# Kernel optimization log

Hardware: AMD Instinct MI355X
Metric: run time of the kernel (lower is better)

Reference implementation:

```python
import jax, jax.numpy as jnp
import numpy as np

N_NODES = 100000
N_EDGES = 3200000
N_GRAPHS = 4096
N_REL = 5
N_BASES = 4
HID = 32


def setup_inputs() -> dict:
    key = jax.random.key(0)
    ks = jax.random.split(key, 32)
    inp = {}
    inp['x'] = jax.random.normal(ks[0], (N_NODES, 4), dtype=jnp.float32)
    inp['edge_index'] = jax.random.randint(ks[1], (2, N_EDGES), 0, N_NODES, dtype=jnp.int64)
    inp['edge_type'] = jax.random.randint(ks[2], (N_EDGES,), 0, N_REL, dtype=jnp.int64)
    inp['user_idx'] = jax.random.randint(ks[3], (N_GRAPHS,), 0, N_NODES, dtype=jnp.int64)
    inp['item_idx'] = jax.random.randint(ks[4], (N_GRAPHS,), 0, N_NODES, dtype=jnp.int64)
    k = 5
    for l in range(4):
        in_c = 4 if l == 0 else HID
        inp[f'basis{l}'] = jax.random.normal(ks[k], (N_BASES, in_c, HID), dtype=jnp.float32) * 0.1; k += 1
        inp[f'comp{l}'] = jax.random.normal(ks[k], (N_REL, N_BASES), dtype=jnp.float32) * 0.5; k += 1
        inp[f'root{l}'] = jax.random.normal(ks[k], (in_c, HID), dtype=jnp.float32) * 0.1; k += 1
        inp[f'bias{l}'] = jax.random.normal(ks[k], (HID,), dtype=jnp.float32) * 0.01; k += 1
    inp['w1'] = jax.random.normal(ks[k], (256, 128), dtype=jnp.float32) * 0.05; k += 1
    inp['b1'] = jnp.zeros((128,), dtype=jnp.float32)
    inp['w2'] = jax.random.normal(ks[k], (128, 1), dtype=jnp.float32) * 0.05; k += 1
    inp['b2'] = jnp.zeros((1,), dtype=jnp.float32)
    return inp


def _rgcn_layer(x, src, key5, inv_cnt, basis, comp, root, bias, n_nodes):
    # mean-aggregate raw source features per (dst, relation): [N, R, in]
    agg = jax.ops.segment_sum(x[src], key5, num_segments=n_nodes * N_REL)
    agg = agg.reshape(n_nodes, N_REL, -1) * inv_cnt
    # basis-decomposed relation weights: W_r = sum_b comp[r,b] * basis[b]
    w = jnp.einsum('rb,bio->rio', comp, basis)  # [R, in, out]
    return jnp.einsum('nri,rio->no', agg, w) + x @ root + bias


def reference(x, edge_index, edge_type, user_idx, item_idx,
              basis0, comp0, root0, bias0,
              basis1, comp1, root1, bias1,
              basis2, comp2, root2, bias2,
              basis3, comp3, root3, bias3,
              w1, b1, w2, b2):
    n_nodes = x.shape[0]
    src, dst = edge_index[0], edge_index[1]
    key5 = dst * N_REL + edge_type  # combined (dst, relation) segment id
    cnt = jax.ops.segment_sum(jnp.ones_like(edge_type, dtype=x.dtype), key5,
                              num_segments=n_nodes * N_REL)
    inv_cnt = (1.0 / jnp.maximum(cnt, 1.0)).reshape(n_nodes, N_REL, 1)
    params = [(basis0, comp0, root0, bias0), (basis1, comp1, root1, bias1),
              (basis2, comp2, root2, bias2), (basis3, comp3, root3, bias3)]
    out = x
    hs = []
    for (basis, comp, root, bias) in params:
        out = jnp.tanh(_rgcn_layer(out, src, key5, inv_cnt, basis, comp, root, bias, n_nodes))
        hs.append(out)
    h = jnp.concatenate(hs, axis=1)            # [N, 128]
    g = jnp.concatenate([h[user_idx], h[item_idx]], axis=1)  # [B, 256]
    z = jax.nn.relu(g @ w1 + b1)
    return (z @ w2 + b2)[:, 0]
```

## Files before the change

kernel.cpp:

```cpp
#include <hip/hip_runtime.h>
#include <hip/hip_bf16.h>
#include <hip/hip_fp16.h>

#define N_NODES 100000
#define N_EDGES 3200000
#define N_GRAPHS 4096
#define N_REL 5
#define N_BASES 4
#define HID 32
#define SEG (N_NODES*N_REL)
#define DUMMY N_NODES

#define NBUCK 392
#define BCAP  10240
#define PBCAP 15360
#define NKEY  1280
#define PTILE 4096

typedef _Float16 half8 __attribute__((ext_vector_type(8)));
typedef float floatx4 __attribute__((ext_vector_type(4)));

static __global__ __launch_bounds__(256) void k_part(const int* __restrict__ ei,
                                                     const int* __restrict__ et,
                                                     int* __restrict__ gcur,
                                                     unsigned long long* __restrict__ part) {
    __shared__ unsigned long long stage[PTILE];
    __shared__ int hist[NBUCK];
    __shared__ int lofs[NBUCK];
    __shared__ int lbase[NBUCK];
    __shared__ int sscan[256];
    int t = threadIdx.x;
    int e0 = blockIdx.x * PTILE;
    int tile_n = N_EDGES - e0; if (tile_n > PTILE) tile_n = PTILE;

    for (int k = t; k < NBUCK; k += 256) hist[k] = 0;
    __syncthreads();
    int src[16], bkt[16], lkey[16];
#pragma unroll
    for (int j = 0; j < 16; j++) {
        int e = e0 + j * 256 + t;
        if (e < N_EDGES) {
            int s = ei[e];
            int d = ei[N_EDGES + e];
            int r = et[e];
            src[j] = s; bkt[j] = d >> 8; lkey[j] = ((d & 255) * 5) + r;
            atomicAdd(&hist[bkt[j]], 1);
        } else bkt[j] = -1;
    }
    __syncthreads();
    int h0 = (2 * t     < NBUCK) ? hist[2 * t]     : 0;
    int h1 = (2 * t + 1 < NBUCK) ? hist[2 * t + 1] : 0;
    int s2 = h0 + h1;
    sscan[t] = s2;
    __syncthreads();
    for (int off = 1; off < 256; off <<= 1) {
        int xv = (t >= off) ? sscan[t - off] : 0;
        __syncthreads();
        sscan[t] += xv;
        __syncthreads();
    }
    int excl = sscan[t] - s2;
    if (2 * t     < NBUCK) lofs[2 * t]     = excl;
    if (2 * t + 1 < NBUCK) lofs[2 * t + 1] = excl + h0;
    for (int k = t; k < NBUCK; k += 256) lbase[k] = atomicAdd(&gcur[k], hist[k]);
    __syncthreads();
    for (int k = t; k < NBUCK; k += 256) hist[k] = 0;
    __syncthreads();
#pragma unroll
    for (int j = 0; j < 16; j++) {
        if (bkt[j] >= 0) {
            int rank = atomicAdd(&hist[bkt[j]], 1);
            stage[lofs[bkt[j]] + rank] =
                ((unsigned long long)(unsigned)((bkt[j] << 16) | lkey[j]) << 32)
                | (unsigned)src[j];
        }
    }
    __syncthreads();
    for (int i = t; i < tile_n; i += 256) {
        unsigned long long u = stage[i];
        unsigned hi = (unsigned)(u >> 32);
        int bb = hi >> 16;
        unsigned long long lk = hi & 0xFFFFu;
        int pos = lbase[bb] + (i - lofs[bb]);
        if (pos < BCAP)
            part[(size_t)bb * BCAP + pos] = (lk << 32) | (u & 0xffffffffULL);
    }
}

static __global__ __launch_bounds__(1024) void k_bsort(const unsigned long long* __restrict__ part,
                                                       const int* __restrict__ gcur,
                                                       int* __restrict__ offs,
                                                       int* __restrict__ cnt,
                                                       int* __restrict__ srcs) {
    __shared__ int lhist[NKEY];
    __shared__ int lscan[NKEY];
    __shared__ int sscan[256];
    __shared__ int lsrc[PBCAP];
    int b = blockIdx.x;
    int t = threadIdx.x;
    int n = gcur[b]; if (n > BCAP) n = BCAP;
    const unsigned long long* reg = part + (size_t)b * BCAP;

    for (int k = t; k < NKEY; k += 1024) lhist[k] = 0;
    __syncthreads();
    for (int i = t; i < n; i += 1024)
        atomicAdd(&lhist[(int)(reg[i] >> 32)], 1);
    __syncthreads();

    int loc[5]; int s5 = 0;
    if (t < 256) {
#pragma unroll
        for (int j = 0; j < 5; j++) { loc[j] = s5; s5 += (lhist[t * 5 + j] + 7) & ~7; }
        sscan[t] = s5;
    }
    __syncthreads();
    for (int off = 1; off < 256; off <<= 1) {
        int x = (t >= off && t < 256) ? sscan[t - off] : 0;
        __syncthreads();
        if (t < 256) sscan[t] += x;
        __syncthreads();
    }
    if (t < 256) {
        int excl = sscan[t] - s5;
#pragma unroll
        for (int j = 0; j < 5; j++) lscan[t * 5 + j] = excl + loc[j];
    }
    __syncthreads();
    int ptot = sscan[255]; if (ptot > PBCAP) ptot = PBCAP;
    int pout = ptot + 16; if (pout > PBCAP) pout = PBCAP;

    int base = b * PBCAP;
    if (t < 256) {
#pragma unroll
        for (int j = 0; j < 5; j++) {
            int k = t * 5 + j;
            int segid = b * NKEY + k;
            if (segid < SEG) {
                cnt[segid]  = lhist[k];
                offs[segid] = base + lscan[k];
            }
        }
    }
    __syncthreads();
    for (int k = t; k < NKEY; k += 1024) lhist[k] = 0;
    for (int i = t; i < pout; i += 1024) lsrc[i] = DUMMY;
    __syncthreads();
    for (int i = t; i < n; i += 1024) {
        unsigned long long u = reg[i];
        int k = (int)(u >> 32);
        int pos = lscan[k] + atomicAdd(&lhist[k], 1);
        if (pos < PBCAP) lsrc[pos] = (int)(u & 0xffffffffULL);
    }
    __syncthreads();
    for (int i = t; i < pout; i += 1024) srcs[base + i] = lsrc[i];
}

static __global__ __launch_bounds__(256) void k_pad(const float* __restrict__ x,
                                                    __half* __restrict__ ht0,
                                                    __half* __restrict__ ht1,
                                                    __half* __restrict__ ht2,
                                                    __half* __restrict__ ht3,
                                                    __half* __restrict__ ht4,
                                                    int* __restrict__ srcs) {
    int tid = blockIdx.x * 256 + threadIdx.x;
    if (tid < (N_NODES + 1) * 32) {
        int nd = tid >> 5, ii = tid & 31;
        float v = (nd < N_NODES && ii < 4) ? x[(nd << 2) + ii] : 0.f;
        ht0[tid] = __float2half(v);
    } else {
        int r = tid - (N_NODES + 1) * 32;
        if (r < 128) {
            __half* hp = (r < 32) ? ht1 : (r < 64) ? ht2 : (r < 96) ? ht3 : ht4;
            hp[N_NODES * 32 + (r & 31)] = __float2half(0.f);
        } else if (r < 144) srcs[NBUCK * PBCAP + (r - 128)] = DUMMY;
    }
}

static __global__ __launch_bounds__(256) void k_wprepB(
    const float* __restrict__ ba0, const float* __restrict__ ro0,
    const float* __restrict__ ba1, const float* __restrict__ ro1,
    const float* __restrict__ ba2, const float* __restrict__ ro2,
    const float* __restrict__ ba3, const float* __restrict__ ro3,
    __half* __restrict__ Wb) {
    int idx = blockIdx.x * 256 + threadIdx.x;
    int j    = idx & 7;
    int lane = (idx >> 3) & 63;
    int tile = (idx >> 9) & 1;
    int ls   = idx >> 10;
    int l    = ls / 5;
    int s    = ls - l * 5;
    const float* basis = (l == 0) ? ba0 : (l == 1) ? ba1 : (l == 2) ? ba2 : ba3;
    const float* root  = (l == 0) ? ro0 : (l == 1) ? ro1 : (l == 2) ? ro2 : ro3;
    int in_c = (l == 0) ? 4 : HID;
    int k = s * 32 + ((lane >> 4) << 3) + j;
    int o = tile * 16 + (lane & 15);
    float v;
    if (k < 128) {
        int b = k >> 5, ii = k & 31;
        v = (ii < in_c) ? basis[(b * in_c + ii) * HID + o] : 0.f;
    } else {
        int ii = k - 128;
        v = (ii < in_c) ? root[ii * HID + o] : 0.f;
    }
    Wb[idx] = __float2half(v);
}

static __global__ __launch_bounds__(256) void k_wprepM(const float* __restrict__ w1,
                                                       __half* __restrict__ Wm) {
    int idx = blockIdx.x * 256 + threadIdx.x;
    int j    = idx & 7;
    int lane = (idx >> 3) & 63;
    int s    = (idx >> 9) & 7;
    int tile = idx >> 12;
    int k = s * 32 + ((lane >> 4) << 3) + j;
    int o = tile * 16 + (lane & 15);
    Wm[idx] = __float2half(w1[k * 128 + o]);
}

static __global__ __launch_bounds__(256, 8) void k_layer(
    const __half2* __restrict__ tab, const int* __restrict__ offs,
    const int* __restrict__ cnt, const int* __restrict__ srcs,
    const float* __restrict__ comp, const __half* __restrict__ Wbl,
    const float* __restrict__ bias, __half* __restrict__ hout) {
    __shared__ __align__(16) __half sAgg16[16 * 176];
    int t = threadIdx.x;
    int wave = t >> 6, q = (t >> 4) & 3, p = t & 15;

    float4 cw0 = *(const float4*)(comp + 0);
    float4 cw1 = *(const float4*)(comp + 4);
    float4 cw2 = *(const float4*)(comp + 8);
    float4 cw3 = *(const float4*)(comp + 12);
    float4 cw4 = *(const float4*)(comp + 16);

    int n = blockIdx.x * 16 + wave * 4 + q;
    int s5 = n * N_REL;
    int oo[6], cc[5];
#pragma unroll
    for (int r = 0; r < 5; r++) { oo[r] = offs[s5 + r]; cc[r] = cnt[s5 + r]; }
    oo[5] = oo[4] + ((cc[4] + 7) & ~7);

    __half2 selfh = tab[n * 16 + p];
    float a0x = 0.f, a0y = 0.f, a1x = 0.f, a1y = 0.f;
    float a2x = 0.f, a2y = 0.f, a3x = 0.f, a3y = 0.f;

#pragma unroll
    for (int r = 0; r < 5; r++) {
        int pR = oo[r], pr = oo[r + 1] - pR;
        const int* sp = srcs + pR;
        int4 e0 = *(const int4*)(sp);
        int4 e1 = *(const int4*)(sp + 4);
        __half2 g0 = tab[e0.x * 16 + p], g1 = tab[e0.y * 16 + p];
        __half2 g2 = tab[e0.z * 16 + p], g3 = tab[e0.w * 16 + p];
        __half2 g4 = tab[e1.x * 16 + p], g5 = tab[e1.y * 16 + p];
        __half2 g6 = tab[e1.z * 16 + p], g7 = tab[e1.w * 16 + p];
        __half2 sb = __hadd2(__hadd2(__hadd2(g0, g1), __hadd2(g2, g3)),
                             __hadd2(__hadd2(g4, g5), __hadd2(g6, g7)));
        float2 bf = __half22float2(sb);
        float Sx = bf.x, Sy = bf.y;
        for (int s8 = 8; s8 < pr; s8 += 8) {
            int4 f0 = *(const int4*)(sp + s8);
            int4 f1 = *(const int4*)(sp + s8 + 4);
            __half2 h0 = tab[f0.x * 16 + p], h1 = tab[f0.y * 16 + p];
            __half2 h2 = tab[f0.z * 16 + p], h3 = tab[f0.w * 16 + p];
            __half2 h4 = tab[f1.x * 16 + p], h5 = tab[f1.y * 16 + p];
            __half2 h6 = tab[f1.z * 16 + p], h7 = tab[f1.w * 16 + p];
            __half2 rb = __hadd2(__hadd2(__hadd2(h0, h1), __hadd2(h2, h3)),
                                 __hadd2(__hadd2(h4, h5), __hadd2(h6, h7)));
            float2 rf = __half22float2(rb);
            Sx += rf.x; Sy += rf.y;
        }
        int cr = cc[r];
        float ic = (cr > 0) ? __builtin_amdgcn_rcpf((float)cr) : 0.f;
        float scx = Sx * ic, scy = Sy * ic;
        float4 cw = (r == 0) ? cw0 : (r == 1) ? cw1 : (r == 2) ? cw2
                  : (r == 3) ? cw3 : cw4;
        a0x += cw.x * scx; a0y += cw.x * scy;
        a1x += cw.y * scx; a1y += cw.y * scy;
        a2x += cw.z * scx; a2y += cw.z * scy;
        a3x += cw.w * scx; a3y += cw.w * scy;
    }
    int nl = wave * 4 + q;
    __half2* row = (__half2*)(sAgg16 + nl * 176);
    row[p]      = __float22half2_rn(make_float2(a0x, a0y));
    row[16 + p] = __float22half2_rn(make_float2(a1x, a1y));
    row[32 + p] = __float22half2_rn(make_float2(a2x, a2y));
    row[48 + p] = __float22half2_rn(make_float2(a3x, a3y));
    row[64 + p] = selfh;
    __syncthreads();

    if (wave < 2) {
        int lane = t & 63;
        floatx4 acc = {0.f, 0.f, 0.f, 0.f};
        const __half* aBase = sAgg16 + (lane & 15) * 176 + ((lane >> 4) << 3);
        const __half* bBase = Wbl + wave * 512 + lane * 8;
#pragma unroll
        for (int s = 0; s < 5; s++) {
            half8 a = *(const half8*)(aBase + s * 32);
            half8 b = *(const half8*)(bBase + s * 1024);
            acc = __builtin_amdgcn_mfma_f32_16x16x32_f16(a, b, acc, 0, 0, 0);
        }
        int o = wave * 16 + (lane & 15);
        float bi = bias[o];
#pragma unroll
        for (int r = 0; r < 4; r++) {
            int node = blockIdx.x * 16 + ((lane >> 4) << 2) + r;
            hout[node * 32 + o] = __float2half(tanhf(acc[r] + bi));
        }
    }
}

static __global__ __launch_bounds__(256) void k_mlp(
    const __half* __restrict__ h1, const __half* __restrict__ h2,
    const __half* __restrict__ h3, const __half* __restrict__ h4,
    const int* __restrict__ uidx, const int* __restrict__ iidx,
    const __half* __restrict__ Wm, const float* __restrict__ b1,
    const float* __restrict__ w2, const float* __restrict__ b2,
    float* __restrict__ out) {
    __shared__ __align__(16) __half sg[16 * 264];
    __shared__ float sacc[4][16];
    int t = threadIdx.x, wave = t >> 6, lane = t & 63;
    int g0 = blockIdx.x * 16;
    int lt = lane >> 4, lp = lane & 15;
    const __half* htab = (lt == 0) ? h1 : (lt == 1) ? h2 : (lt == 2) ? h3 : h4;
#pragma unroll
    for (int gg2 = 0; gg2 < 4; gg2++) {
        int gg = wave * 4 + gg2;
        int g = g0 + gg;
        int u = uidx[g], it = iidx[g];
        __half2* dst = (__half2*)(sg + gg * 264);
        dst[lt * 16 + lp]      = ((const __half2*)(htab + u * 32))[lp];
        dst[64 + lt * 16 + lp] = ((const __half2*)(htab + it * 32))[lp];
    }
    __syncthreads();
    floatx4 acc0 = {0.f, 0.f, 0.f, 0.f}, acc1 = {0.f, 0.f, 0.f, 0.f};
    const __half* aBase = sg + (lane & 15) * 264 + ((lane >> 4) << 3);
    const __half* bB0 = Wm + (wave * 2 + 0) * 4096 + lane * 8;
    const __half* bB1 = Wm + (wave * 2 + 1) * 4096 + lane * 8;
#pragma unroll
    for (int s = 0; s < 8; s++) {
        half8 a  = *(const half8*)(aBase + s * 32);
        half8 f0 = *(const half8*)(bB0 + s * 512);
        half8 f1 = *(const half8*)(bB1 + s * 512);
        acc0 = __builtin_amdgcn_mfma_f32_16x16x32_f16(a, f0, acc0, 0, 0, 0);
        acc1 = __builtin_amdgcn_mfma_f32_16x16x32_f16(a, f1, acc1, 0, 0, 0);
    }
    int o0 = wave * 32 + (lane & 15);
    int o1 = o0 + 16;
    float b10 = b1[o0], b11 = b1[o1], w20 = w2[o0], w21 = w2[o1];
#pragma unroll
    for (int r = 0; r < 4; r++) {
        float z0 = fmaxf(acc0[r] + b10, 0.f);
        float z1 = fmaxf(acc1[r] + b11, 0.f);
        float v = z0 * w20 + z1 * w21;
#pragma unroll
        for (int off = 1; off < 16; off <<= 1) v += __shfl_xor(v, off);
        if ((lane & 15) == 0) sacc[wave][((lane >> 4) << 2) + r] = v;
    }
    __syncthreads();
    if (t < 16)
        out[g0 + t] = sacc[0][t] + sacc[1][t] + sacc[2][t] + sacc[3][t] + b2[0];
}

extern "C" void kernel_launch(void* const* d_in, const int* in_sizes, int n_in,
                              void* d_out, int out_size, void* d_ws, size_t ws_size,
                              hipStream_t stream) {
    const float* x  = (const float*)d_in[0];
    const int*   ei = (const int*)d_in[1];
    const int*   et = (const int*)d_in[2];
    const int*   ui = (const int*)d_in[3];
    const int*   ii = (const int*)d_in[4];
    const float* w1 = (const float*)d_in[21];
    const float* b1 = (const float*)d_in[22];
    const float* w2 = (const float*)d_in[23];
    const float* b2 = (const float*)d_in[24];

    char* ws = (char*)d_ws;
    if (ws_size < 92167680UL) return;
    int*    gcur = (int*)(ws + 0);
    int*    offs = (int*)(ws + 2048);
    int*    cnt  = (int*)(ws + 2002176);
    int*    srcs = (int*)(ws + 4002304);
    __half* Wb   = (__half*)(ws + 28086912);
    __half* Wm   = (__half*)(ws + 28127872);
    __half* ht0  = (__half*)(ws + 28193536);
    __half* ht1  = (__half*)(ws + 34593664);
    __half* ht2  = (__half*)(ws + 40993792);
    __half* ht3  = (__half*)(ws + 47393920);
    __half* ht4  = (__half*)(ws + 53794048);
    unsigned long long* part = (unsigned long long*)(ws + 34593664);

    hipMemsetAsync(gcur, 0, NBUCK * 4, stream);

    k_part<<<(N_EDGES + PTILE - 1) / PTILE, 256, 0, stream>>>(ei, et, gcur, part);
    k_bsort<<<NBUCK, 1024, 0, stream>>>(part, gcur, offs, cnt, srcs);
    k_pad<<<12501, 256, 0, stream>>>(x, ht0, ht1, ht2, ht3, ht4, srcs);
    k_wprepB<<<80, 256, 0, stream>>>(
        (const float*)d_in[5],  (const float*)d_in[7],
        (const float*)d_in[9],  (const float*)d_in[11],
        (const float*)d_in[13], (const float*)d_in[15],
        (const float*)d_in[17], (const float*)d_in[19], Wb);
    k_wprepM<<<128, 256, 0, stream>>>(w1, Wm);

    __half* tabs[5] = {ht0, ht1, ht2, ht3, ht4};
    for (int l = 0; l < 4; l++) {
        const float* comp = (const float*)d_in[6 + 4 * l];
        const float* bias = (const float*)d_in[8 + 4 * l];
        k_layer<<<6250, 256, 0, stream>>>((const __half2*)tabs[l], offs, cnt,
                                          srcs, comp, Wb + l * 5120, bias,
                                          tabs[l + 1]);
    }
    k_mlp<<<256, 256, 0, stream>>>(ht1, ht2, ht3, ht4, ui, ii, Wm, b1, w2, b2,
                                   (float*)d_out);
}
```

Baseline: 345.1 us.

## Precompute relation weights and gather half8 rows per lane with wider MFMA tiles

The weight-prep kernel now folds the basis coefficients into per-relation weight matrices (5 relations plus root, K=192). The per-edge comp mixing is gone from the layer kernel, which instead stores raw per-relation means in shared memory. The gather now uses 4 lanes per node, each loading 16 bytes (half8) instead of 16 lanes loading half2, and each block covers 64 nodes. All four waves run MFMA with two output tiles across 6 K-steps. This gives fewer, wider memory transactions per edge and less FMA work, at the cost of more MFMA work, larger shared memory and lower occupancy.

```diff
diff --git a/kernel.cpp b/kernel.cpp
--- a/kernel.cpp
+++ b/kernel.cpp
@@ -16,6 +16,9 @@
 #define PBCAP 15360
 #define NKEY  1280
 #define PTILE 4096
+
+#define KDIM 192
+#define ASTR 208
 
 typedef _Float16 half8 __attribute__((ext_vector_type(8)));
 typedef float floatx4 __attribute__((ext_vector_type(4)));
@@ -177,30 +180,35 @@
 }
 
 static __global__ __launch_bounds__(256) void k_wprepB(
-    const float* __restrict__ ba0, const float* __restrict__ ro0,
-    const float* __restrict__ ba1, const float* __restrict__ ro1,
-    const float* __restrict__ ba2, const float* __restrict__ ro2,
-    const float* __restrict__ ba3, const float* __restrict__ ro3,
+    const float* __restrict__ ba0, const float* __restrict__ co0, const float* __restrict__ ro0,
+    const float* __restrict__ ba1, const float* __restrict__ co1, const float* __restrict__ ro1,
+    const float* __restrict__ ba2, const float* __restrict__ co2, const float* __restrict__ ro2,
+    const float* __restrict__ ba3, const float* __restrict__ co3, const float* __restrict__ ro3,
     __half* __restrict__ Wb) {
     int idx = blockIdx.x * 256 + threadIdx.x;
     int j    = idx & 7;
     int lane = (idx >> 3) & 63;
     int tile = (idx >> 9) & 1;
     int ls   = idx >> 10;
-    int l    = ls / 5;
-    int s    = ls - l * 5;
+    int l    = ls / 6;
+    int s    = ls - l * 6;
     const float* basis = (l == 0) ? ba0 : (l == 1) ? ba1 : (l == 2) ? ba2 : ba3;
+    const float* comp  = (l == 0) ? co0 : (l == 1) ? co1 : (l == 2) ? co2 : co3;
     const float* root  = (l == 0) ? ro0 : (l == 1) ? ro1 : (l == 2) ? ro2 : ro3;
     int in_c = (l == 0) ? 4 : HID;
-    int k = s * 32 + ((lane >> 4) << 3) + j;
+    int d = ((lane >> 4) << 3) + j;
     int o = tile * 16 + (lane & 15);
-    float v;
-    if (k < 128) {
-        int b = k >> 5, ii = k & 31;
-        v = (ii < in_c) ? basis[(b * in_c + ii) * HID + o] : 0.f;
-    } else {
-        int ii = k - 128;
-        v = (ii < in_c) ? root[ii * HID + o] : 0.f;
+    float v = 0.f;
+    if (d < in_c) {
+        if (s < 5) {
+            float acc = 0.f;
+#pragma unroll
+            for (int b = 0; b < N_BASES; b++)
+                acc += comp[s * N_BASES + b] * basis[(b * in_c + d) * HID + o];
+            v = acc;
+        } else {
+            v = root[d * HID + o];
+        }
     }
     Wb[idx] = __float2half(v);
 }
@@ -217,94 +225,86 @@
     Wm[idx] = __float2half(w1[k * 128 + o]);
 }
 
-static __global__ __launch_bounds__(256, 8) void k_layer(
-    const __half2* __restrict__ tab, const int* __restrict__ offs,
+static __global__ __launch_bounds__(256, 6) void k_layer(
+    const __half* __restrict__ tab, const int* __restrict__ offs,
     const int* __restrict__ cnt, const int* __restrict__ srcs,
-    const float* __restrict__ comp, const __half* __restrict__ Wbl,
-    const float* __restrict__ bias, __half* __restrict__ hout) {
-    __shared__ __align__(16) __half sAgg16[16 * 176];
+    const __half* __restrict__ Wbl, const float* __restrict__ bias,
+    __half* __restrict__ hout) {
+    __shared__ __align__(16) __half sAgg[64 * ASTR];
     int t = threadIdx.x;
-    int wave = t >> 6, q = (t >> 4) & 3, p = t & 15;
-
-    float4 cw0 = *(const float4*)(comp + 0);
-    float4 cw1 = *(const float4*)(comp + 4);
-    float4 cw2 = *(const float4*)(comp + 8);
-    float4 cw3 = *(const float4*)(comp + 12);
-    float4 cw4 = *(const float4*)(comp + 16);
-
-    int n = blockIdx.x * 16 + wave * 4 + q;
-    int s5 = n * N_REL;
-    int oo[6], cc[5];
-#pragma unroll
-    for (int r = 0; r < 5; r++) { oo[r] = offs[s5 + r]; cc[r] = cnt[s5 + r]; }
-    oo[5] = oo[4] + ((cc[4] + 7) & ~7);
-
-    __half2 selfh = tab[n * 16 + p];
-    float a0x = 0.f, a0y = 0.f, a1x = 0.f, a1y = 0.f;
-    float a2x = 0.f, a2y = 0.f, a3x = 0.f, a3y = 0.f;
-
+    int wave = t >> 6, lane = t & 63;
+    int nsub = lane >> 2, cp = lane & 3;
+    int nl = wave * 16 + nsub;
+    int n = blockIdx.x * 64 + nl;
+    int nn = (n < N_NODES) ? n : (N_NODES - 1);
+    const half8* tab8 = (const half8*)tab;
+
+    int s5 = nn * N_REL;
+    int o0 = offs[s5];
+    int cc[5];
+#pragma unroll
+    for (int r = 0; r < 5; r++) cc[r] = cnt[s5 + r];
+
+    __half* row = sAgg + nl * ASTR;
+    half8 selfv = tab8[nn * 4 + cp];
+    *(half8*)(row + 160 + cp * 8) = selfv;
+
+    int orun = o0;
 #pragma unroll
     for (int r = 0; r < 5; r++) {
-        int pR = oo[r], pr = oo[r + 1] - pR;
-        const int* sp = srcs + pR;
+        int cr = cc[r];
+        int pr = (cr + 7) & ~7;
+        const int* sp = srcs + orun;
         int4 e0 = *(const int4*)(sp);
         int4 e1 = *(const int4*)(sp + 4);
-        __half2 g0 = tab[e0.x * 16 + p], g1 = tab[e0.y * 16 + p];
-        __half2 g2 = tab[e0.z * 16 + p], g3 = tab[e0.w * 16 + p];
-        __half2 g4 = tab[e1.x * 16 + p], g5 = tab[e1.y * 16 + p];
-        __half2 g6 = tab[e1.z * 16 + p], g7 = tab[e1.w * 16 + p];
-        __half2 sb = __hadd2(__hadd2(__hadd2(g0, g1), __hadd2(g2, g3)),
-                             __hadd2(__hadd2(g4, g5), __hadd2(g6, g7)));
-        float2 bf = __half22float2(sb);
-        float Sx = bf.x, Sy = bf.y;
+        half8 g0 = tab8[e0.x * 4 + cp], g1 = tab8[e0.y * 4 + cp];
+        half8 g2 = tab8[e0.z * 4 + cp], g3 = tab8[e0.w * 4 + cp];
+        half8 g4 = tab8[e1.x * 4 + cp], g5 = tab8[e1.y * 4 + cp];
+        half8 g6 = tab8[e1.z * 4 + cp], g7 = tab8[e1.w * 4 + cp];
+        half8 sb = ((g0 + g1) + (g2 + g3)) + ((g4 + g5) + (g6 + g7));
+        float S0 = (float)sb[0], S1 = (float)sb[1], S2 = (float)sb[2], S3 = (float)sb[3];
+        float S4 = (float)sb[4], S5 = (float)sb[5], S6 = (float)sb[6], S7 = (float)sb[7];
         for (int s8 = 8; s8 < pr; s8 += 8) {
             int4 f0 = *(const int4*)(sp + s8);
             int4 f1 = *(const int4*)(sp + s8 + 4);
-            __half2 h0 = tab[f0.x * 16 + p], h1 = tab[f0.y * 16 + p];
-            __half2 h2 = tab[f0.z * 16 + p], h3 = tab[f0.w * 16 + p];
-            __half2 h4 = tab[f1.x * 16 + p], h5 = tab[f1.y * 16 + p];
-            __half2 h6 = tab[f1.z * 16 + p], h7 = tab[f1.w * 16 + p];
-            __half2 rb = __hadd2(__hadd2(__hadd2(h0, h1), __hadd2(h2, h3)),
-                                 __hadd2(__hadd2(h4, h5), __hadd2(h6, h7)));
-            float2 rf = __half22float2(rb);
-            Sx += rf.x; Sy += rf.y;
+            half8 h0 = tab8[f0.x * 4 + cp], h1 = tab8[f0.y * 4 + cp];
+            half8 h2 = tab8[f0.z * 4 + cp], h3 = tab8[f0.w * 4 + cp];
+            half8 h4 = tab8[f1.x * 4 + cp], h5 = tab8[f1.y * 4 + cp];
+            half8 h6 = tab8[f1.z * 4 + cp], h7 = tab8[f1.w * 4 + cp];
+            half8 rb = ((h0 + h1) + (h2 + h3)) + ((h4 + h5) + (h6 + h7));
+            S0 += (float)rb[0]; S1 += (float)rb[1]; S2 += (float)rb[2]; S3 += (float)rb[3];
+            S4 += (float)rb[4]; S5 += (float)rb[5]; S6 += (float)rb[6]; S7 += (float)rb[7];
         }
-        int cr = cc[r];
         float ic = (cr > 0) ? __builtin_amdgcn_rcpf((float)cr) : 0.f;
-        float scx = Sx * ic, scy = Sy * ic;
-        float4 cw = (r == 0) ? cw0 : (r == 1) ? cw1 : (r == 2) ? cw2
-                  : (r == 3) ? cw3 : cw4;
-        a0x += cw.x * scx; a0y += cw.x * scy;
-        a1x += cw.y * scx; a1y += cw.y * scy;
-        a2x += cw.z * scx; a2y += cw.z * scy;
-        a3x += cw.w * scx; a3y += cw.w * scy;
-    }
-    int nl = wave * 4 + q;
-    __half2* row = (__half2*)(sAgg16 + nl * 176);
-    row[p]      = __float22half2_rn(make_float2(a0x, a0y));
-    row[16 + p] = __float22half2_rn(make_float2(a1x, a1y));
-    row[32 + p] = __float22half2_rn(make_float2(a2x, a2y));
-    row[48 + p] = __float22half2_rn(make_float2(a3x, a3y));
-    row[64 + p] = selfh;
-    __syncthreads();
-
-    if (wave < 2) {
-        int lane = t & 63;
-        floatx4 acc = {0.f, 0.f, 0.f, 0.f};
-        const __half* aBase = sAgg16 + (lane & 15) * 176 + ((lane >> 4) << 3);
-        const __half* bBase = Wbl + wave * 512 + lane * 8;
-#pragma unroll
-        for (int s = 0; s < 5; s++) {
-            half8 a = *(const half8*)(aBase + s * 32);
-            half8 b = *(const half8*)(bBase + s * 1024);
-            acc = __builtin_amdgcn_mfma_f32_16x16x32_f16(a, b, acc, 0, 0, 0);
-        }
-        int o = wave * 16 + (lane & 15);
-        float bi = bias[o];
-#pragma unroll
-        for (int r = 0; r < 4; r++) {
-            int node = blockIdx.x * 16 + ((lane >> 4) << 2) + r;
-            hout[node * 32 + o] = __float2half(tanhf(acc[r] + bi));
+        half8 u;
+        u[0] = (_Float16)(S0 * ic); u[1] = (_Float16)(S1 * ic);
+        u[2] = (_Float16)(S2 * ic); u[3] = (_Float16)(S3 * ic);
+        u[4] = (_Float16)(S4 * ic); u[5] = (_Float16)(S5 * ic);
+        u[6] = (_Float16)(S6 * ic); u[7] = (_Float16)(S7 * ic);
+        *(half8*)(row + r * 32 + cp * 8) = u;
+        orun += pr;
+    }
+    __syncthreads();
+
+    floatx4 acc0 = {0.f, 0.f, 0.f, 0.f}, acc1 = {0.f, 0.f, 0.f, 0.f};
+    const __half* aBase = sAgg + (wave * 16 + (lane & 15)) * ASTR + ((lane >> 4) << 3);
+    const __half* bBase = Wbl + lane * 8;
+#pragma unroll
+    for (int s = 0; s < 6; s++) {
+        half8 a  = *(const half8*)(aBase + s * 32);
+        half8 f0 = *(const half8*)(bBase + (s * 2 + 0) * 512);
+        half8 f1 = *(const half8*)(bBase + (s * 2 + 1) * 512);
+        acc0 = __builtin_amdgcn_mfma_f32_16x16x32_f16(a, f0, acc0, 0, 0, 0);
+        acc1 = __builtin_amdgcn_mfma_f32_16x16x32_f16(a, f1, acc1, 0, 0, 0);
+    }
+    int oc = lane & 15;
+    float bi0 = bias[oc], bi1 = bias[16 + oc];
+#pragma unroll
+    for (int r = 0; r < 4; r++) {
+        int node = blockIdx.x * 64 + wave * 16 + ((lane >> 4) << 2) + r;
+        if (node < N_NODES) {
+            hout[node * 32 + oc]      = __float2half(tanhf(acc0[r] + bi0));
+            hout[node * 32 + 16 + oc] = __float2half(tanhf(acc1[r] + bi1));
         }
     }
 }
@@ -381,33 +381,31 @@
     int*    cnt  = (int*)(ws + 2002176);
     int*    srcs = (int*)(ws + 4002304);
     __half* Wb   = (__half*)(ws + 28086912);
-    __half* Wm   = (__half*)(ws + 28127872);
-    __half* ht0  = (__half*)(ws + 28193536);
-    __half* ht1  = (__half*)(ws + 34593664);
-    __half* ht2  = (__half*)(ws + 40993792);
-    __half* ht3  = (__half*)(ws + 47393920);
-    __half* ht4  = (__half*)(ws + 53794048);
-    unsigned long long* part = (unsigned long long*)(ws + 34593664);
+    __half* Wm   = (__half*)(ws + 28136064);
+    __half* ht0  = (__half*)(ws + 28201600);
+    __half* ht1  = (__half*)(ws + 34601728);
+    __half* ht2  = (__half*)(ws + 41001856);
+    __half* ht3  = (__half*)(ws + 47401984);
+    __half* ht4  = (__half*)(ws + 53802112);
+    unsigned long long* part = (unsigned long long*)(ws + 34601728);
 
     hipMemsetAsync(gcur, 0, NBUCK * 4, stream);
 
     k_part<<<(N_EDGES + PTILE - 1) / PTILE, 256, 0, stream>>>(ei, et, gcur, part);
     k_bsort<<<NBUCK, 1024, 0, stream>>>(part, gcur, offs, cnt, srcs);
     k_pad<<<12501, 256, 0, stream>>>(x, ht0, ht1, ht2, ht3, ht4, srcs);
-    k_wprepB<<<80, 256, 0, stream>>>(
-        (const float*)d_in[5],  (const float*)d_in[7],
-        (const float*)d_in[9],  (const float*)d_in[11],
-        (const float*)d_in[13], (const float*)d_in[15],
-        (const float*)d_in[17], (const float*)d_in[19], Wb);
+    k_wprepB<<<96, 256, 0, stream>>>(
+        (const float*)d_in[5],  (const float*)d_in[6],  (const float*)d_in[7],
+        (const float*)d_in[9],  (const float*)d_in[10], (const float*)d_in[11],
+        (const float*)d_in[13], (const float*)d_in[14], (const float*)d_in[15],
+        (const float*)d_in[17], (const float*)d_in[18], (const float*)d_in[19], Wb);
     k_wprepM<<<128, 256, 0, stream>>>(w1, Wm);
 
     __half* tabs[5] = {ht0, ht1, ht2, ht3, ht4};
     for (int l = 0; l < 4; l++) {
-        const float* comp = (const float*)d_in[6 + 4 * l];
         const float* bias = (const float*)d_in[8 + 4 * l];
-        k_layer<<<6250, 256, 0, stream>>>((const __half2*)tabs[l], offs, cnt,
-                                          srcs, comp, Wb + l * 5120, bias,
-                                          tabs[l + 1]);
+        k_layer<<<(N_NODES + 63) / 64, 256, 0, stream>>>(
+            tabs[l], offs, cnt, srcs, Wb + l * 6144, bias, tabs[l + 1]);
     }
     k_mlp<<<256, 256, 0, stream>>>(ht1, ht2, ht3, ht4, ui, ii, Wm, b1, w2, b2,
                                    (float*)d_out);
```

Measured after the change: 361.3 us. +4.7%, slower.
